# Performance work log

Measured on AMD Instinct MI355X. Metric: run time of the kernel, lower is better.

The kernel has to match this reference:

```python
import jax, jax.numpy as jnp
import numpy as np

N_NODES = 100000
N_EDGES = 6400000
D_FEAT = 128

def setup_inputs() -> dict:
    key = jax.random.key(0)
    k1, k2, k3 = jax.random.split(key, 3)
    h = jax.random.normal(k1, (N_NODES, D_FEAT), dtype=jnp.float32)
    src = jax.random.randint(k2, (N_EDGES,), 0, N_NODES, dtype=jnp.int64)
    dst = jax.random.randint(k3, (N_EDGES,), 0, N_NODES, dtype=jnp.int64)
    return {"h": h, "src": src, "dst": dst}

def reference(h, src, dst):
    N = h.shape[0]
    pos = h[:, 0]                                  # [N] scalar position per node
    # per-edge message: |pos_src - pos_dst|
    dist = jnp.abs(pos[src] - pos[dst])            # [E]
    # segment-mean over incoming edges at each dst node
    s = jax.ops.segment_sum(dist, dst, num_segments=N)                  # [N]
    cnt = jax.ops.segment_sum(jnp.ones_like(dist), dst, num_segments=N)  # [N] in-degree
    h_dst = s / jnp.maximum(cnt, 1.0)              # zero-in-degree nodes -> 0 (DGL default)
    return jnp.stack([pos, h_dst], axis=1)         # [N, 2]
```

## Files before the change

### kernel.cpp

```cpp
#include <hip/hip_runtime.h>

#define D_FEAT 128
#define NBINS_MAX 10
#define BIN_SIZE 10000
#define PB 4000
#define PB_THREADS 256
#define CAP 256
#define CAP_SHIFT 8
#define SBB 50
#define SEGS (PB / SBB)
#define SC_THREADS 1024
#define DIST_SCALE 1024.0f
#define INV_DIST_SCALE (1.0f / 1024.0f)

__global__ __launch_bounds__(PB_THREADS, 8) void prep_kernel(
        const int* __restrict__ src, const int* __restrict__ dst,
        const float* __restrict__ h, float* __restrict__ pos,
        unsigned int* __restrict__ pv2, unsigned int* __restrict__ cnts,
        int n_edges, int n_nodes, int nbins, int chunk) {
    __shared__ unsigned int cursor[NBINS_MAX];
    const int b = blockIdx.x;
    const int t = threadIdx.x;
    if (t < nbins) cursor[t] = 0u;
    __syncthreads();

    {
        int share = (n_nodes + gridDim.x - 1) / gridDim.x;
        int lo = b * share;
        int hi = min(lo + share, n_nodes);
        for (int i = lo + t; i < hi; i += PB_THREADS)
            pos[i] = h[(size_t)i * D_FEAT];
    }

    const long base = (long)b * chunk;
    long lim = (long)n_edges - base;
    if (lim > chunk) lim = chunk;
    if (lim < 0) lim = 0;

#define PREP_ONE(dd, ss)                                                        \
    {                                                                           \
        unsigned int d = (unsigned int)(dd);                                    \
        unsigned int bin = d / BIN_SIZE;                                        \
        unsigned int drel = d - bin * BIN_SIZE;                                 \
        unsigned int slot = atomicAdd(&cursor[bin], 1u);                        \
        if (slot < CAP)                                                         \
            pv2[(((size_t)bin * PB + b) << CAP_SHIFT) + slot] =                 \
                ((unsigned int)(ss) << 14) | drel;                              \
    }

    int k4 = (int)(lim & ~3L);
    for (int k = t * 4; k < k4; k += PB_THREADS * 4) {
        int4 d4 = *(const int4*)(dst + base + k);
        int4 s4 = *(const int4*)(src + base + k);
        PREP_ONE(d4.x, s4.x);
        PREP_ONE(d4.y, s4.y);
        PREP_ONE(d4.z, s4.z);
        PREP_ONE(d4.w, s4.w);
    }
    for (long k = k4 + t; k < lim; k += PB_THREADS) {
        PREP_ONE(dst[base + k], src[base + k]);
    }
#undef PREP_ONE
    __syncthreads();
    if (t < nbins) {
        unsigned int c = cursor[t];
        cnts[t * PB + b] = c < CAP ? c : CAP;
    }
}

__global__ __launch_bounds__(SC_THREADS) void scatter_kernel(
        const unsigned int* __restrict__ pv2, const unsigned int* __restrict__ cnts,
        const float* __restrict__ pos, unsigned int* __restrict__ part,
        int n_nodes) {
    __shared__ unsigned int lacc[BIN_SIZE];
    __shared__ float pos_lds[BIN_SIZE];
    __shared__ unsigned int cl[SEGS];
    const int bx = blockIdx.x;
    const int bin = bx / SBB;
    const int j = bx - bin * SBB;
    const int bin_lo = bin * BIN_SIZE;
    const int bin_n = min(BIN_SIZE, n_nodes - bin_lo);
    const int t = threadIdx.x;

    if (t < SEGS) cl[t] = cnts[bin * PB + j * SEGS + t];
    for (int k = t; k < bin_n; k += SC_THREADS) {
        lacc[k] = 0u;
        pos_lds[k] = pos[bin_lo + k];
    }
    __syncthreads();

#define SC_BODY(vv)                                                             \
    {                                                                           \
        float a = pos[(vv) >> 14];                                              \
        unsigned int r = (vv) & 0x3FFFu;                                        \
        unsigned int f = min((unsigned int)(fabsf(a - pos_lds[r]) * DIST_SCALE + 0.5f), 16383u); \
        atomicAdd(&lacc[r], (1u << 24) | f);                                    \
    }

    const unsigned int* pj = pv2 + (((size_t)bin * PB + (size_t)j * SEGS) << CAP_SHIFT);
    const int TOT = SEGS * CAP;
    for (int idx = t * 8; idx < TOT; idx += SC_THREADS * 8) {
        int seg = idx >> CAP_SHIFT;
        int slot = idx & (CAP - 1);
        int cnt = (int)cl[seg];
        const unsigned int* p = pj + ((size_t)seg << CAP_SHIFT);
        if (slot + 8 <= cnt) {
            uint4 va = *(const uint4*)(p + slot);
            uint4 vb = *(const uint4*)(p + slot + 4);
            float a0 = pos[va.x >> 14]; float a1 = pos[va.y >> 14];
            float a2 = pos[va.z >> 14]; float a3 = pos[va.w >> 14];
            float a4 = pos[vb.x >> 14]; float a5 = pos[vb.y >> 14];
            float a6 = pos[vb.z >> 14]; float a7 = pos[vb.w >> 14];
            unsigned int r0 = va.x & 0x3FFFu, r1 = va.y & 0x3FFFu;
            unsigned int r2 = va.z & 0x3FFFu, r3 = va.w & 0x3FFFu;
            unsigned int r4 = vb.x & 0x3FFFu, r5 = vb.y & 0x3FFFu;
            unsigned int r6 = vb.z & 0x3FFFu, r7 = vb.w & 0x3FFFu;
            unsigned int f0 = min((unsigned int)(fabsf(a0 - pos_lds[r0]) * DIST_SCALE + 0.5f), 16383u);
            unsigned int f1 = min((unsigned int)(fabsf(a1 - pos_lds[r1]) * DIST_SCALE + 0.5f), 16383u);
            unsigned int f2 = min((unsigned int)(fabsf(a2 - pos_lds[r2]) * DIST_SCALE + 0.5f), 16383u);
            unsigned int f3 = min((unsigned int)(fabsf(a3 - pos_lds[r3]) * DIST_SCALE + 0.5f), 16383u);
            unsigned int f4 = min((unsigned int)(fabsf(a4 - pos_lds[r4]) * DIST_SCALE + 0.5f), 16383u);
            unsigned int f5 = min((unsigned int)(fabsf(a5 - pos_lds[r5]) * DIST_SCALE + 0.5f), 16383u);
            unsigned int f6 = min((unsigned int)(fabsf(a6 - pos_lds[r6]) * DIST_SCALE + 0.5f), 16383u);
            unsigned int f7 = min((unsigned int)(fabsf(a7 - pos_lds[r7]) * DIST_SCALE + 0.5f), 16383u);
            atomicAdd(&lacc[r0], (1u << 24) | f0);
            atomicAdd(&lacc[r1], (1u << 24) | f1);
            atomicAdd(&lacc[r2], (1u << 24) | f2);
            atomicAdd(&lacc[r3], (1u << 24) | f3);
            atomicAdd(&lacc[r4], (1u << 24) | f4);
            atomicAdd(&lacc[r5], (1u << 24) | f5);
            atomicAdd(&lacc[r6], (1u << 24) | f6);
            atomicAdd(&lacc[r7], (1u << 24) | f7);
        } else if (slot < cnt) {
            for (int q = slot; q < cnt && q < slot + 8; ++q) SC_BODY(p[q]);
        }
    }
#undef SC_BODY
    __syncthreads();

    unsigned int* slice = part + (size_t)j * n_nodes + bin_lo;
    for (int k = t; k < bin_n; k += SC_THREADS) slice[k] = lacc[k];
}

__global__ void merge_kernel(const float* __restrict__ pos,
                             const unsigned int* __restrict__ part,
                             float* __restrict__ out, int n_nodes) {
    int i0 = (blockIdx.x * blockDim.x + threadIdx.x) * 4;
    if (i0 + 4 <= n_nodes) {
        unsigned int c0 = 0, c1 = 0, c2 = 0, c3 = 0;
        unsigned int s0 = 0, s1 = 0, s2 = 0, s3 = 0;
        for (int b = 0; b < SBB; ++b) {
            uint4 p = *(const uint4*)(part + (size_t)b * n_nodes + i0);
            c0 += p.x >> 24; s0 += p.x & 0x00FFFFFFu;
            c1 += p.y >> 24; s1 += p.y & 0x00FFFFFFu;
            c2 += p.z >> 24; s2 += p.z & 0x00FFFFFFu;
            c3 += p.w >> 24; s3 += p.w & 0x00FFFFFFu;
        }
        float4 ps = *(const float4*)(pos + i0);
        float4 oa, ob;
        oa.x = ps.x; oa.y = ((float)s0 * INV_DIST_SCALE) / fmaxf((float)c0, 1.0f);
        oa.z = ps.y; oa.w = ((float)s1 * INV_DIST_SCALE) / fmaxf((float)c1, 1.0f);
        ob.x = ps.z; ob.y = ((float)s2 * INV_DIST_SCALE) / fmaxf((float)c2, 1.0f);
        ob.z = ps.w; ob.w = ((float)s3 * INV_DIST_SCALE) / fmaxf((float)c3, 1.0f);
        ((float4*)out)[(i0 >> 1)] = oa;
        ((float4*)out)[(i0 >> 1) + 1] = ob;
    } else {
        for (int i = i0; i < n_nodes; ++i) {
            unsigned int cnt = 0, sum = 0;
            for (int b = 0; b < SBB; ++b) {
                unsigned int p = part[(size_t)b * n_nodes + i];
                cnt += p >> 24;
                sum += p & 0x00FFFFFFu;
            }
            float2 o;
            o.x = pos[i];
            o.y = ((float)sum * INV_DIST_SCALE) / fmaxf((float)cnt, 1.0f);
            ((float2*)out)[i] = o;
        }
    }
}

__global__ void fb_init(const float* __restrict__ h, float* __restrict__ pos,
                        unsigned long long* __restrict__ acc, int n) {
    int i = blockIdx.x * blockDim.x + threadIdx.x;
    if (i < n) { pos[i] = h[(size_t)i * D_FEAT]; acc[i] = 0ull; }
}
__global__ void fb_edge(const int* __restrict__ src, const int* __restrict__ dst,
                        const float* __restrict__ pos,
                        unsigned long long* __restrict__ acc, int n_edges) {
    int stride = gridDim.x * blockDim.x;
    for (int i = blockIdx.x * blockDim.x + threadIdx.x; i < n_edges; i += stride) {
        float dist = fabsf(pos[src[i]] - pos[dst[i]]);
        unsigned int fx = (unsigned int)(dist * 262144.0f + 0.5f);
        atomicAdd(&acc[dst[i]], (1ull << 32) | (unsigned long long)fx);
    }
}
__global__ void fb_final(const float* __restrict__ pos,
                         const unsigned long long* __restrict__ acc,
                         float* __restrict__ out, int n) {
    int i = blockIdx.x * blockDim.x + threadIdx.x;
    if (i < n) {
        unsigned long long v = acc[i];
        unsigned int cnt = (unsigned int)(v >> 32);
        float s = (float)(unsigned int)(v & 0xffffffffull) * (1.0f / 262144.0f);
        float2 o; o.x = pos[i]; o.y = s / fmaxf((float)cnt, 1.0f);
        ((float2*)out)[i] = o;
    }
}

extern "C" void kernel_launch(void* const* d_in, const int* in_sizes, int n_in,
                              void* d_out, int out_size, void* d_ws, size_t ws_size,
                              hipStream_t stream) {
    const float* h = (const float*)d_in[0];
    const int* src = (const int*)d_in[1];
    const int* dst = (const int*)d_in[2];
    float* out = (float*)d_out;

    int n_nodes = in_sizes[0] / D_FEAT;
    int n_edges = in_sizes[1];

    int chunk = (n_edges + PB - 1) / PB;
    int nbins = (n_nodes + BIN_SIZE - 1) / BIN_SIZE;
    size_t pos_bytes  = ((size_t)n_nodes * 4 + 255) & ~(size_t)255;
    size_t pv2_bytes  = (((size_t)nbins * PB << CAP_SHIFT) * 4 + 255) & ~(size_t)255;
    size_t cnts_bytes = ((size_t)nbins * PB * 4 + 255) & ~(size_t)255;
    size_t part_bytes = (size_t)SBB * n_nodes * 4;
    bool fast_ok = (ws_size >= pos_bytes + pv2_bytes + cnts_bytes + part_bytes) &&
                   (n_nodes <= (1 << 17)) && (nbins <= NBINS_MAX) &&
                   ((size_t)chunk * 10 <= (size_t)CAP * nbins * 7);

    int block = 256;
    int ngrid = (n_nodes + block - 1) / block;

    if (fast_ok) {
        char* w = (char*)d_ws;
        float* pos = (float*)w;                          w += pos_bytes;
        unsigned int* pv2 = (unsigned int*)w;            w += pv2_bytes;
        unsigned int* cnts = (unsigned int*)w;           w += cnts_bytes;
        unsigned int* part = (unsigned int*)w;
        prep_kernel<<<PB, PB_THREADS, 0, stream>>>(src, dst, h, pos, pv2, cnts,
                                                   n_edges, n_nodes, nbins, chunk);
        scatter_kernel<<<nbins * SBB, SC_THREADS, 0, stream>>>(pv2, cnts, pos,
                                                               part, n_nodes);
        int mgrid = (n_nodes + block * 4 - 1) / (block * 4);
        merge_kernel<<<mgrid, block, 0, stream>>>(pos, part, out, n_nodes);
    } else {
        float* pos = (float*)d_ws;
        unsigned long long* acc = (unsigned long long*)((char*)d_ws + pos_bytes);
        fb_init<<<ngrid, block, 0, stream>>>(h, pos, acc, n_nodes);
        fb_edge<<<(n_edges + block - 1) / block, block, 0, stream>>>(src, dst, pos, acc, n_edges);
        fb_final<<<ngrid, block, 0, stream>>>(pos, acc, out, n_nodes);
    }
}
```

Before: 176.4 us.

## Bin edges by source and destination block to stage both positions in LDS

Result: slower. 273.3 us (+54.9%).

```diff
diff --git a/kernel.cpp b/kernel.cpp
--- a/kernel.cpp
+++ b/kernel.cpp
@@ -1,13 +1,14 @@
 #include <hip/hip_runtime.h>
 
 #define D_FEAT 128
-#define NBINS_MAX 10
-#define BIN_SIZE 10000
-#define PB 4000
+#define NB 16
+#define BIN_SIZE 6400
+#define BSHIFT 13
+#define PB 2048
 #define PB_THREADS 256
-#define CAP 256
-#define CAP_SHIFT 8
-#define SBB 50
+#define CAP 64
+#define CAP_SHIFT 6
+#define SBB 32
 #define SEGS (PB / SBB)
 #define SC_THREADS 1024
 #define DIST_SCALE 1024.0f
@@ -18,10 +19,11 @@
         const float* __restrict__ h, float* __restrict__ pos,
         unsigned int* __restrict__ pv2, unsigned int* __restrict__ cnts,
         int n_edges, int n_nodes, int nbins, int chunk) {
-    __shared__ unsigned int cursor[NBINS_MAX];
+    __shared__ unsigned int cursor[NB * NB];
     const int b = blockIdx.x;
     const int t = threadIdx.x;
-    if (t < nbins) cursor[t] = 0u;
+    const int cells = nbins * nbins;
+    for (int c = t; c < cells; c += PB_THREADS) cursor[c] = 0u;
     __syncthreads();
 
     {
@@ -40,12 +42,14 @@
 #define PREP_ONE(dd, ss)                                                        \
     {                                                                           \
         unsigned int d = (unsigned int)(dd);                                    \
-        unsigned int bin = d / BIN_SIZE;                                        \
-        unsigned int drel = d - bin * BIN_SIZE;                                 \
-        unsigned int slot = atomicAdd(&cursor[bin], 1u);                        \
+        unsigned int s = (unsigned int)(ss);                                    \
+        unsigned int db = d / BIN_SIZE;                                         \
+        unsigned int sb = s / BIN_SIZE;                                         \
+        unsigned int cell = sb * (unsigned int)nbins + db;                      \
+        unsigned int rec = ((s - sb * BIN_SIZE) << BSHIFT) | (d - db * BIN_SIZE); \
+        unsigned int slot = atomicAdd(&cursor[cell], 1u);                       \
         if (slot < CAP)                                                         \
-            pv2[(((size_t)bin * PB + b) << CAP_SHIFT) + slot] =                 \
-                ((unsigned int)(ss) << 14) | drel;                              \
+            pv2[(((size_t)cell * PB + b) << CAP_SHIFT) + slot] = rec;           \
     }
 
     int k4 = (int)(lim & ~3L);
@@ -62,84 +66,69 @@
     }
 #undef PREP_ONE
     __syncthreads();
-    if (t < nbins) {
-        unsigned int c = cursor[t];
-        cnts[t * PB + b] = c < CAP ? c : CAP;
+    for (int c = t; c < cells; c += PB_THREADS) {
+        unsigned int v = cursor[c];
+        cnts[(size_t)c * PB + b] = v < CAP ? v : CAP;
     }
 }
 
 __global__ __launch_bounds__(SC_THREADS) void scatter_kernel(
         const unsigned int* __restrict__ pv2, const unsigned int* __restrict__ cnts,
         const float* __restrict__ pos, unsigned int* __restrict__ part,
-        int n_nodes) {
+        int n_nodes, int nbins) {
     __shared__ unsigned int lacc[BIN_SIZE];
-    __shared__ float pos_lds[BIN_SIZE];
-    __shared__ unsigned int cl[SEGS];
+    __shared__ float pos_d[BIN_SIZE];
+    __shared__ float pos_s[BIN_SIZE];
+    __shared__ unsigned int cl_sb[SEGS];
     const int bx = blockIdx.x;
-    const int bin = bx / SBB;
-    const int j = bx - bin * SBB;
-    const int bin_lo = bin * BIN_SIZE;
-    const int bin_n = min(BIN_SIZE, n_nodes - bin_lo);
+    const int dbin = bx >> 5;
+    const int j = bx & (SBB - 1);
+    const int dlo = dbin * BIN_SIZE;
+    const int dn = min(BIN_SIZE, n_nodes - dlo);
     const int t = threadIdx.x;
 
-    if (t < SEGS) cl[t] = cnts[bin * PB + j * SEGS + t];
-    for (int k = t; k < bin_n; k += SC_THREADS) {
+    for (int k = t; k < dn; k += SC_THREADS) {
         lacc[k] = 0u;
-        pos_lds[k] = pos[bin_lo + k];
-    }
-    __syncthreads();
+        pos_d[k] = pos[dlo + k];
+    }
+
+    for (int sb = 0; sb < nbins; ++sb) {
+        const int slo = sb * BIN_SIZE;
+        const int sn = min(BIN_SIZE, n_nodes - slo);
+        __syncthreads();
+        if (t < SEGS) cl_sb[t] = cnts[(size_t)(sb * nbins + dbin) * PB + j * SEGS + t];
+        for (int k = t; k < sn; k += SC_THREADS) pos_s[k] = pos[slo + k];
+        __syncthreads();
 
 #define SC_BODY(vv)                                                             \
     {                                                                           \
-        float a = pos[(vv) >> 14];                                              \
-        unsigned int r = (vv) & 0x3FFFu;                                        \
-        unsigned int f = min((unsigned int)(fabsf(a - pos_lds[r]) * DIST_SCALE + 0.5f), 16383u); \
-        atomicAdd(&lacc[r], (1u << 24) | f);                                    \
-    }
-
-    const unsigned int* pj = pv2 + (((size_t)bin * PB + (size_t)j * SEGS) << CAP_SHIFT);
-    const int TOT = SEGS * CAP;
-    for (int idx = t * 8; idx < TOT; idx += SC_THREADS * 8) {
-        int seg = idx >> CAP_SHIFT;
-        int slot = idx & (CAP - 1);
-        int cnt = (int)cl[seg];
-        const unsigned int* p = pj + ((size_t)seg << CAP_SHIFT);
-        if (slot + 8 <= cnt) {
-            uint4 va = *(const uint4*)(p + slot);
-            uint4 vb = *(const uint4*)(p + slot + 4);
-            float a0 = pos[va.x >> 14]; float a1 = pos[va.y >> 14];
-            float a2 = pos[va.z >> 14]; float a3 = pos[va.w >> 14];
-            float a4 = pos[vb.x >> 14]; float a5 = pos[vb.y >> 14];
-            float a6 = pos[vb.z >> 14]; float a7 = pos[vb.w >> 14];
-            unsigned int r0 = va.x & 0x3FFFu, r1 = va.y & 0x3FFFu;
-            unsigned int r2 = va.z & 0x3FFFu, r3 = va.w & 0x3FFFu;
-            unsigned int r4 = vb.x & 0x3FFFu, r5 = vb.y & 0x3FFFu;
-            unsigned int r6 = vb.z & 0x3FFFu, r7 = vb.w & 0x3FFFu;
-            unsigned int f0 = min((unsigned int)(fabsf(a0 - pos_lds[r0]) * DIST_SCALE + 0.5f), 16383u);
-            unsigned int f1 = min((unsigned int)(fabsf(a1 - pos_lds[r1]) * DIST_SCALE + 0.5f), 16383u);
-            unsigned int f2 = min((unsigned int)(fabsf(a2 - pos_lds[r2]) * DIST_SCALE + 0.5f), 16383u);
-            unsigned int f3 = min((unsigned int)(fabsf(a3 - pos_lds[r3]) * DIST_SCALE + 0.5f), 16383u);
-            unsigned int f4 = min((unsigned int)(fabsf(a4 - pos_lds[r4]) * DIST_SCALE + 0.5f), 16383u);
-            unsigned int f5 = min((unsigned int)(fabsf(a5 - pos_lds[r5]) * DIST_SCALE + 0.5f), 16383u);
-            unsigned int f6 = min((unsigned int)(fabsf(a6 - pos_lds[r6]) * DIST_SCALE + 0.5f), 16383u);
-            unsigned int f7 = min((unsigned int)(fabsf(a7 - pos_lds[r7]) * DIST_SCALE + 0.5f), 16383u);
-            atomicAdd(&lacc[r0], (1u << 24) | f0);
-            atomicAdd(&lacc[r1], (1u << 24) | f1);
-            atomicAdd(&lacc[r2], (1u << 24) | f2);
-            atomicAdd(&lacc[r3], (1u << 24) | f3);
-            atomicAdd(&lacc[r4], (1u << 24) | f4);
-            atomicAdd(&lacc[r5], (1u << 24) | f5);
-            atomicAdd(&lacc[r6], (1u << 24) | f6);
-            atomicAdd(&lacc[r7], (1u << 24) | f7);
-        } else if (slot < cnt) {
-            for (int q = slot; q < cnt && q < slot + 8; ++q) SC_BODY(p[q]);
+        unsigned int sr = (vv) >> BSHIFT;                                       \
+        unsigned int dr = (vv) & ((1u << BSHIFT) - 1u);                         \
+        float diff = pos_s[sr] - pos_d[dr];                                     \
+        unsigned int f = min((unsigned int)(fabsf(diff) * DIST_SCALE + 0.5f), 16383u); \
+        atomicAdd(&lacc[dr], (1u << 24) | f);                                   \
+    }
+        const unsigned int* pj = pv2 +
+            (((size_t)(sb * nbins + dbin) * PB + (size_t)j * SEGS) << CAP_SHIFT);
+        const int TOT = SEGS * CAP;
+        for (int idx = t * 4; idx < TOT; idx += SC_THREADS * 4) {
+            int seg = idx >> CAP_SHIFT;
+            int slot = idx & (CAP - 1);
+            int cnt = (int)cl_sb[seg];
+            const unsigned int* p = pj + ((size_t)seg << CAP_SHIFT);
+            if (slot + 4 <= cnt) {
+                uint4 v = *(const uint4*)(p + slot);
+                SC_BODY(v.x); SC_BODY(v.y); SC_BODY(v.z); SC_BODY(v.w);
+            } else if (slot < cnt) {
+                for (int q = slot; q < cnt && q < slot + 4; ++q) SC_BODY(p[q]);
+            }
         }
-    }
 #undef SC_BODY
+    }
     __syncthreads();
 
-    unsigned int* slice = part + (size_t)j * n_nodes + bin_lo;
-    for (int k = t; k < bin_n; k += SC_THREADS) slice[k] = lacc[k];
+    unsigned int* slice = part + (size_t)j * n_nodes + dlo;
+    for (int k = t; k < dn; k += SC_THREADS) slice[k] = lacc[k];
 }
 
 __global__ void merge_kernel(const float* __restrict__ pos,
@@ -221,13 +210,14 @@
 
     int chunk = (n_edges + PB - 1) / PB;
     int nbins = (n_nodes + BIN_SIZE - 1) / BIN_SIZE;
+    int cells = nbins * nbins;
     size_t pos_bytes  = ((size_t)n_nodes * 4 + 255) & ~(size_t)255;
-    size_t pv2_bytes  = (((size_t)nbins * PB << CAP_SHIFT) * 4 + 255) & ~(size_t)255;
-    size_t cnts_bytes = ((size_t)nbins * PB * 4 + 255) & ~(size_t)255;
+    size_t pv2_bytes  = (((size_t)cells * PB << CAP_SHIFT) * 4 + 255) & ~(size_t)255;
+    size_t cnts_bytes = ((size_t)cells * PB * 4 + 255) & ~(size_t)255;
     size_t part_bytes = (size_t)SBB * n_nodes * 4;
     bool fast_ok = (ws_size >= pos_bytes + pv2_bytes + cnts_bytes + part_bytes) &&
-                   (n_nodes <= (1 << 17)) && (nbins <= NBINS_MAX) &&
-                   ((size_t)chunk * 10 <= (size_t)CAP * nbins * 7);
+                   (nbins <= NB) &&
+                   ((size_t)chunk * 2 <= (size_t)CAP * cells);
 
     int block = 256;
     int ngrid = (n_nodes + block - 1) / block;
@@ -241,7 +231,7 @@
         prep_kernel<<<PB, PB_THREADS, 0, stream>>>(src, dst, h, pos, pv2, cnts,
                                                    n_edges, n_nodes, nbins, chunk);
         scatter_kernel<<<nbins * SBB, SC_THREADS, 0, stream>>>(pv2, cnts, pos,
-                                                               part, n_nodes);
+                                                               part, n_nodes, nbins);
         int mgrid = (n_nodes + block * 4 - 1) / (block * 4);
         merge_kernel<<<mgrid, block, 0, stream>>>(pos, part, out, n_nodes);
     } else {
```
